# Optimization experiments

Hardware: AMD Instinct MI355X
Metric: run time of the kernel (lower is better)

Reference implementation:

```python
import jax, jax.numpy as jnp
import numpy as np

NUM_HEADS = 16
ROPE_THETA = 10000.0


def setup_inputs() -> dict:
    key = jax.random.key(0)
    k1, k2, k3 = jax.random.split(key, 3)
    B, T, C = 2, 2048, 1024
    x = jax.random.normal(k1, (B, T, C), dtype=jnp.float32)
    w_qkv = jax.random.normal(k2, (3 * C, C), dtype=jnp.float32) * 0.02
    w_out = jax.random.normal(k3, (C, C), dtype=jnp.float32) * 0.02
    return {"x": x, "w_qkv": w_qkv, "w_out": w_out}


def _apply_rope(x, cos, sin):
    # x: (B, H, T, D); interleaved complex pairs: (x[...,2i], x[...,2i+1])
    B, H, T, D = x.shape
    xp = x.reshape(B, H, T, D // 2, 2)
    xr, xi = xp[..., 0], xp[..., 1]
    # cos/sin: (T, D//2) broadcast over (B, H)
    out_r = xr * cos - xi * sin
    out_i = xr * sin + xi * cos
    return jnp.stack([out_r, out_i], axis=-1).reshape(B, H, T, D)


def reference(x, w_qkv, w_out):
    B, T, C = x.shape
    H = NUM_HEADS
    D = C // H
    scale = 1.0 / np.sqrt(D).astype(np.float32)

    qkv = x @ w_qkv.T                      # (B, T, 3C)
    q, k, v = jnp.split(qkv, 3, axis=-1)

    def to_heads(t):
        return t.reshape(B, T, H, D).transpose(0, 2, 1, 3)  # (B, H, T, D)

    q, k, v = to_heads(q), to_heads(k), to_heads(v)

    # RoPE frequencies: freqs[t, j] = t / theta^(2j/D)
    inv_freq = 1.0 / (ROPE_THETA ** (jnp.arange(0, D, 2, dtype=jnp.float32) / D))
    freqs = jnp.arange(T, dtype=jnp.float32)[:, None] * inv_freq[None, :]  # (T, D//2)
    cos, sin = jnp.cos(freqs), jnp.sin(freqs)

    q = _apply_rope(q, cos, sin)
    k = _apply_rope(k, cos, sin)

    att = jnp.einsum('bhqd,bhkd->bhqk', q, k) * scale   # (B, H, T, T)
    causal = jnp.tril(jnp.ones((T, T), dtype=bool))
    att = jnp.where(causal[None, None], att, -jnp.inf)
    att = jax.nn.softmax(att, axis=-1)
    # dropout p=0.0 (eval) -> identity

    out = jnp.einsum('bhqk,bhkd->bhqd', att, v)          # (B, H, T, D)
    out = out.transpose(0, 2, 1, 3).reshape(B, T, C)
    return out @ w_out.T
```

## Files before the change

kernel.cpp:

```cpp
#include <hip/hip_runtime.h>
#include <hip/hip_bf16.h>
#include <math.h>

#define DEV __device__ __forceinline__

typedef float  floatx4 __attribute__((ext_vector_type(4)));
typedef short  bf16x8  __attribute__((ext_vector_type(8)));
typedef short  bf16x4  __attribute__((ext_vector_type(4)));

typedef __attribute__((address_space(1))) void gvoid;
typedef __attribute__((address_space(3))) void lvoid;

static constexpr int Bc = 2, Tc = 2048, Cc = 1024, Hc = 16, Dc = 64;

DEV void gload16(const void* g, void* l) {
    __builtin_amdgcn_global_load_lds((gvoid*)g, (lvoid*)l, 16, 0, 0);
}

__global__ void prep_kernel(const float* __restrict__ xf,
                            const float* __restrict__ wqkvf,
                            const float* __restrict__ woutf,
                            __hip_bfloat16* __restrict__ xb,
                            __hip_bfloat16* __restrict__ wqkvb,
                            __hip_bfloat16* __restrict__ woutb,
                            float* __restrict__ cosT, float* __restrict__ sinT) {
    int gb = blockIdx.x;
    if (gb < 8192) {
        const float* src; __hip_bfloat16* dst; int i;
        if (gb < 4096)      { src = xf;    dst = xb;    i = gb * 256 + threadIdx.x; }
        else if (gb < 7168) { src = wqkvf; dst = wqkvb; i = (gb - 4096) * 256 + threadIdx.x; }
        else                { src = woutf; dst = woutb; i = (gb - 7168) * 256 + threadIdx.x; }
        float4 f = ((const float4*)src)[i];
        union { ushort4 u; __hip_bfloat16 h[4]; } pk;
        pk.h[0] = __float2bfloat16(f.x);
        pk.h[1] = __float2bfloat16(f.y);
        pk.h[2] = __float2bfloat16(f.z);
        pk.h[3] = __float2bfloat16(f.w);
        ((ushort4*)dst)[i] = pk.u;
    } else {
        int i = (gb - 8192) * 256 + threadIdx.x;
        int j = i >> 11, t = i & 2047;
        float invf = powf(10000.0f, -(float)j / 32.0f);
        float f = (float)t * invf;
        cosT[i] = cosf(f);
        sinT[i] = sinf(f);
    }
}

__global__ __launch_bounds__(256, 2) void gemm_qkv(
    const __hip_bfloat16* __restrict__ A,
    const __hip_bfloat16* __restrict__ Bm,
    __hip_bfloat16* __restrict__ qb,
    __hip_bfloat16* __restrict__ kb,
    __hip_bfloat16* __restrict__ vb,
    const float* __restrict__ cosT,
    const float* __restrict__ sinT,
    int K)
{
    __shared__ __align__(16) __hip_bfloat16 SM[2 * 128 * 64];
    __hip_bfloat16* const As = SM;
    __hip_bfloat16* const Bs = SM + 128 * 64;

    const int tid  = threadIdx.x;
    const int lane = tid & 63, wave = tid >> 6;
    const int quad = lane >> 4, cidx = lane & 15;
    const int wm = wave & 1, wn = wave >> 1;
    const int bm = blockIdx.x * 128, bn = blockIdx.y * 128;

    floatx4 acc[4][4] = {};

    for (int k0 = 0; k0 < K; k0 += 64) {
#pragma unroll
        for (int it = 0; it < 4; ++it) {
            int idx = tid + it * 256;
            int r = idx >> 3, cs = idx & 7;
            int cg = cs ^ (r & 7);
            gload16(A  + (size_t)(bm + r) * K + k0 + cg * 8, As + idx * 8);
            gload16(Bm + (size_t)(bn + r) * K + k0 + cg * 8, Bs + idx * 8);
        }
        __syncthreads();
#pragma unroll
        for (int ks = 0; ks < 2; ++ks) {
            bf16x8 af[4], bf[4];
#pragma unroll
            for (int mt = 0; mt < 4; ++mt) {
                int r = wm * 64 + mt * 16 + cidx;
                af[mt] = *(const bf16x8*)(As + (r * 8 + ((ks * 4 + quad) ^ (r & 7))) * 8);
            }
#pragma unroll
            for (int nt = 0; nt < 4; ++nt) {
                int r = wn * 64 + nt * 16 + cidx;
                bf[nt] = *(const bf16x8*)(Bs + (r * 8 + ((ks * 4 + quad) ^ (r & 7))) * 8);
            }
#pragma unroll
            for (int mt = 0; mt < 4; ++mt)
#pragma unroll
                for (int nt = 0; nt < 4; ++nt)
                    acc[mt][nt] = __builtin_amdgcn_mfma_f32_16x16x32_bf16(
                        af[mt], bf[nt], acc[mt][nt], 0, 0, 0);
        }
        __syncthreads();
    }

    if (bn >= 2048) {
#pragma unroll
        for (int nt = 0; nt < 4; ++nt) {
            int n_l = wn * 64 + nt * 16 + cidx;
#pragma unroll
            for (int mt = 0; mt < 4; ++mt)
#pragma unroll
                for (int reg = 0; reg < 4; ++reg) {
                    int m_l = wm * 64 + mt * 16 + quad * 4 + reg;
                    SM[n_l * 128 + (((m_l >> 3) ^ (n_l & 15)) * 8) + (m_l & 7)] =
                        __float2bfloat16(acc[mt][nt][reg]);
                }
        }
        __syncthreads();
        {
            int b = bm >> 11, t0 = bm & 2047;
            int c = tid & 15;
#pragma unroll
            for (int it = 0; it < 8; ++it) {
                int row = it * 16 + (tid >> 4);
                int cc = (bn - 2048) + row;
                int h = cc >> 6, d = cc & 63;
                *(uint4*)(vb + ((size_t)(b * Hc + h) * Dc + d) * Tc + t0 + c * 8) =
                    *(const uint4*)(SM + row * 128 + ((c ^ (row & 15)) * 8));
            }
        }
    } else {
        const float SL2E = 0.125f * 1.44269504088896f;
        const bool isq = (bn < 1024);
#pragma unroll
        for (int nt = 0; nt < 4; ++nt) {
            int n_l = wn * 64 + nt * 16 + cidx;
            int d = n_l & 63, j = d >> 1;
            const float* cp = cosT + j * 2048;
            const float* sp = sinT + j * 2048;
#pragma unroll
            for (int mt = 0; mt < 4; ++mt) {
                int m0 = wm * 64 + mt * 16 + quad * 4;
                int t0 = (bm + m0) & 2047;
                float4 c4 = *(const float4*)(cp + t0);
                float4 s4 = *(const float4*)(sp + t0);
#pragma unroll
                for (int reg = 0; reg < 4; ++reg) {
                    float v = acc[mt][nt][reg];
                    float p = __shfl_xor(v, 1);
                    float cz = ((const float*)&c4)[reg];
                    float sz = ((const float*)&s4)[reg];
                    float o = (d & 1) ? (p * sz + v * cz) : (v * cz - p * sz);
                    if (isq) o *= SL2E;
                    int m_l = m0 + reg;
                    SM[m_l * 128 + (((n_l >> 3) ^ (m_l & 15)) * 8) + (n_l & 7)] =
                        __float2bfloat16(o);
                }
            }
        }
        __syncthreads();
        {
            __hip_bfloat16* dst = isq ? qb : kb;
            const int bnl = bn & 1023;
#pragma unroll
            for (int it = 0; it < 8; ++it) {
                int c = it * 256 + tid;
                int row = c >> 4, s = c & 15;
                int m = bm + row;
                int b = m >> 11, t = m & 2047;
                int h = (bnl >> 6) + (s >> 3);
                int d0 = (s & 7) * 8;
                *(uint4*)(dst + ((size_t)(b * Hc + h) * Tc + t) * Dc + d0) =
                    *(const uint4*)(SM + row * 128 + ((s ^ (row & 15)) * 8));
            }
        }
    }
}

__global__ __launch_bounds__(256, 2) void gemm_out(
    const __hip_bfloat16* __restrict__ A,
    const __hip_bfloat16* __restrict__ Bm,
    float* __restrict__ Cout)
{
    __shared__ __align__(16) __hip_bfloat16 As[64 * 64];
    __shared__ __align__(16) __hip_bfloat16 Bs[128 * 64];

    const int tid  = threadIdx.x;
    const int lane = tid & 63, wave = tid >> 6;
    const int quad = lane >> 4, cidx = lane & 15;
    const int bm = blockIdx.x * 64, bn = blockIdx.y * 128;
    const int K = 1024;

    floatx4 acc[4][2] = {};

    for (int k0 = 0; k0 < K; k0 += 64) {
        int h = k0 >> 6;
#pragma unroll
        for (int it = 0; it < 2; ++it) {
            int idx = tid + it * 256;
            int r = idx >> 3, cs = idx & 7;
            int cg = cs ^ (r & 7);
            int m = bm + r;
            const __hip_bfloat16* src =
                A + ((size_t)((m >> 11) * 16 + h) * 2048 + (m & 2047)) * 64 + cg * 8;
            gload16(src, As + idx * 8);
        }
#pragma unroll
        for (int it = 0; it < 4; ++it) {
            int idx = tid + it * 256;
            int r = idx >> 3, cs = idx & 7;
            int cg = cs ^ (r & 7);
            gload16(Bm + (size_t)(bn + r) * K + k0 + cg * 8, Bs + idx * 8);
        }
        __syncthreads();
#pragma unroll
        for (int ks = 0; ks < 2; ++ks) {
            bf16x8 af[4], bf[2];
#pragma unroll
            for (int mt = 0; mt < 4; ++mt) {
                int r = mt * 16 + cidx;
                af[mt] = *(const bf16x8*)(As + (r * 8 + ((ks * 4 + quad) ^ (r & 7))) * 8);
            }
#pragma unroll
            for (int nt = 0; nt < 2; ++nt) {
                int r = wave * 32 + nt * 16 + cidx;
                bf[nt] = *(const bf16x8*)(Bs + (r * 8 + ((ks * 4 + quad) ^ (r & 7))) * 8);
            }
#pragma unroll
            for (int mt = 0; mt < 4; ++mt)
#pragma unroll
                for (int nt = 0; nt < 2; ++nt)
                    acc[mt][nt] = __builtin_amdgcn_mfma_f32_16x16x32_bf16(
                        af[mt], bf[nt], acc[mt][nt], 0, 0, 0);
        }
        __syncthreads();
    }

#pragma unroll
    for (int mt = 0; mt < 4; ++mt)
#pragma unroll
        for (int nt = 0; nt < 2; ++nt) {
            int n = bn + wave * 32 + nt * 16 + cidx;
#pragma unroll
            for (int reg = 0; reg < 4; ++reg) {
                int m = bm + mt * 16 + quad * 4 + reg;
                Cout[(size_t)m * 1024 + n] = acc[mt][nt][reg];
            }
        }
}

__global__ __launch_bounds__(256, 2) void attn_kernel(
    const __hip_bfloat16* __restrict__ qb,
    const __hip_bfloat16* __restrict__ kb,
    const __hip_bfloat16* __restrict__ vb,
    __hip_bfloat16* __restrict__ ob)
{
    __shared__ __align__(16) __hip_bfloat16 Ks[128 * 64];
    __shared__ __align__(16) __hip_bfloat16 Vt[64 * 128];
    __shared__ __align__(16) __hip_bfloat16 Ps[128 * 64];
    __shared__ float Ls[4][64];

    const int tid  = threadIdx.x;
    const int lane = tid & 63, wave = tid >> 6;
    const int quad = lane >> 4, cidx = lane & 15;
    const int id = blockIdx.x;
    const int xcd = id & 7, s = id >> 3;
    const int bh = xcd * 4 + (s >> 4);
    const int bx = s & 15;
    const size_t plane = (size_t)bh * Tc * Dc;
    const __hip_bfloat16* Vp = vb + plane;
    const __hip_bfloat16* Kp = kb + plane;

    for (int half = 0; half < 2; ++half) {
        const int qt = half ? bx : 31 - bx;
        const int qbase = qt * 64;
        const int ktmax = (qbase + 63) >> 7;

#pragma unroll
        for (int it = 0; it < 2; ++it) {
            int idx = tid + it * 256;
            int r = idx >> 3, cs = idx & 7;
            int cg = cs ^ (r & 7);
            gload16(qb + plane + (size_t)(qbase + r) * 64 + cg * 8, Ks + idx * 8);
        }
        __syncthreads();
        bf16x8 qf[4][2];
#pragma unroll
        for (int mt = 0; mt < 4; ++mt)
#pragma unroll
            for (int ks = 0; ks < 2; ++ks) {
                int r = mt * 16 + cidx;
                qf[mt][ks] = *(const bf16x8*)(Ks + (r * 8 + ((ks * 4 + quad) ^ (r & 7))) * 8);
            }
        __syncthreads();

        floatx4 oaccT[4][4] = {};
        float lsum[4] = {0.f, 0.f, 0.f, 0.f};

        for (int kt = 0; kt <= ktmax; ++kt) {
            bf16x8 kcur[2][2];
#pragma unroll
            for (int nt2 = 0; nt2 < 2; ++nt2)
#pragma unroll
                for (int ks = 0; ks < 2; ++ks)
                    kcur[nt2][ks] = *(const bf16x8*)(
                        Kp + (size_t)(kt * 128 + wave * 32 + nt2 * 16 + cidx) * 64
                           + (ks * 4 + quad) * 8);

#pragma unroll
            for (int it = 0; it < 4; ++it) {
                int idx = tid + it * 256;
                int r = idx >> 4, cs = idx & 15;
                int c = cs ^ (r & 15);
                gload16(Vp + (size_t)r * Tc + kt * 128 + c * 8, Vt + idx * 8);
            }

            floatx4 sacc[4][2] = {};
#pragma unroll
            for (int ks = 0; ks < 2; ++ks)
#pragma unroll
                for (int mt = 0; mt < 4; ++mt)
#pragma unroll
                    for (int nt2 = 0; nt2 < 2; ++nt2)
                        sacc[mt][nt2] = __builtin_amdgcn_mfma_f32_16x16x32_bf16(
                            kcur[nt2][ks], qf[mt][ks], sacc[mt][nt2], 0, 0, 0);

            const bool domask = (kt == ktmax);
            bf16x4 pf[4][2];
#pragma unroll
            for (int mt = 0; mt < 4; ++mt) {
                int q = qbase + mt * 16 + cidx;
#pragma unroll
                for (int nt2 = 0; nt2 < 2; ++nt2) {
#pragma unroll
                    for (int reg = 0; reg < 4; ++reg) {
                        int key = kt * 128 + wave * 32 + nt2 * 16 + quad * 4 + reg;
                        float p = __builtin_amdgcn_exp2f(sacc[mt][nt2][reg]);
                        if (domask && key > q) p = 0.0f;
                        lsum[mt] += p;
                        __hip_bfloat16 hb = __float2bfloat16(p);
                        pf[mt][nt2][reg] = *(const short*)&hb;
                    }
                }
            }

            __syncthreads();

#pragma unroll
            for (int dt = 0; dt < 4; ++dt) {
                int d = dt * 16 + cidx;
#pragma unroll
                for (int ks2 = 0; ks2 < 2; ++ks2) {
                    int chunk = wave * 4 + ks2 * 2 + (quad >> 1);
                    bf16x4 vtf = *(const bf16x4*)(
                        Vt + (d * 16 + (chunk ^ (d & 15))) * 8 + (quad & 1) * 4);
#pragma unroll
                    for (int mt = 0; mt < 4; ++mt)
                        oaccT[mt][dt] = __builtin_amdgcn_mfma_f32_16x16x16bf16_1k(
                            vtf, pf[mt][ks2], oaccT[mt][dt], 0, 0, 0);
                }
            }
            __syncthreads();
        }

#pragma unroll
        for (int off = 16; off < 64; off <<= 1)
#pragma unroll
            for (int mt = 0; mt < 4; ++mt)
                lsum[mt] += __shfl_xor(lsum[mt], off);
        if (quad == 0)
#pragma unroll
            for (int mt = 0; mt < 4; ++mt)
                Ls[wave][mt * 16 + cidx] = lsum[mt];

        if (wave != 0) {
            float* dstw = (wave == 1) ? (float*)Ks : (wave == 2) ? (float*)Vt : (float*)Ps;
#pragma unroll
            for (int mt = 0; mt < 4; ++mt)
#pragma unroll
                for (int dt = 0; dt < 4; ++dt)
                    ((floatx4*)dstw)[(mt * 4 + dt) * 64 + lane] = oaccT[mt][dt];
        }
        __syncthreads();
        if (wave == 0) {
#pragma unroll
            for (int mt = 0; mt < 4; ++mt)
#pragma unroll
                for (int dt = 0; dt < 4; ++dt) {
                    int i = (mt * 4 + dt) * 64 + lane;
                    oaccT[mt][dt] += ((const floatx4*)Ks)[i];
                    oaccT[mt][dt] += ((const floatx4*)Vt)[i];
                    oaccT[mt][dt] += ((const floatx4*)Ps)[i];
                }
#pragma unroll
            for (int mt = 0; mt < 4; ++mt) {
                int q = mt * 16 + cidx;
                float lt = Ls[0][q] + Ls[1][q] + Ls[2][q] + Ls[3][q];
                float inv = 1.0f / lt;
#pragma unroll
                for (int dt = 0; dt < 4; ++dt) {
                    bf16x4 o4;
#pragma unroll
                    for (int reg = 0; reg < 4; ++reg) {
                        __hip_bfloat16 hb = __float2bfloat16(oaccT[mt][dt][reg] * inv);
                        o4[reg] = *(const short*)&hb;
                    }
                    int g = dt * 4 + quad;
                    *(bf16x4*)(Ps + q * 64 + (g ^ (q & 12)) * 4) = o4;
                }
            }
        }
        __syncthreads();
#pragma unroll
        for (int i = 0; i < 2; ++i) {
            int c = tid * 2 + i;
            int row = c >> 3, cp = c & 7;
            *(uint4*)(ob + plane + (size_t)(qbase + row) * 64 + cp * 8) =
                *(const uint4*)(Ps + row * 64 + ((cp * 2) ^ (row & 12)) * 4);
        }
        __syncthreads();
    }
}

extern "C" void kernel_launch(void* const* d_in, const int* in_sizes, int n_in,
                              void* d_out, int out_size, void* d_ws, size_t ws_size,
                              hipStream_t stream) {
    const float* xf = nullptr; const float* wqkvf = nullptr; const float* woutf = nullptr;
    for (int i = 0; i < n_in; ++i) {
        if      (in_sizes[i] == 2 * 2048 * 1024) xf    = (const float*)d_in[i];
        else if (in_sizes[i] == 3 * 1024 * 1024) wqkvf = (const float*)d_in[i];
        else if (in_sizes[i] == 1024 * 1024)     woutf = (const float*)d_in[i];
    }
    float* out = (float*)d_out;

    char* ws = (char*)d_ws;
    const size_t MB = 1024 * 1024;
    __hip_bfloat16* qb    = (__hip_bfloat16*)(ws);
    __hip_bfloat16* kb    = (__hip_bfloat16*)(ws + 8  * MB);
    __hip_bfloat16* vb    = (__hip_bfloat16*)(ws + 16 * MB);
    __hip_bfloat16* ab    = (__hip_bfloat16*)(ws + 24 * MB);
    float* cosT           = (float*)(ws + 32 * MB);
    float* sinT           = (float*)(ws + 32 * MB + 256 * 1024);
    __hip_bfloat16* xb    = (__hip_bfloat16*)(ws + 33 * MB);
    __hip_bfloat16* wqkvb = (__hip_bfloat16*)(ws + 41 * MB);
    __hip_bfloat16* woutb = (__hip_bfloat16*)(ws + 47 * MB);

    prep_kernel<<<dim3(8448), dim3(256), 0, stream>>>(
        xf, wqkvf, woutf, xb, wqkvb, woutb, cosT, sinT);

    gemm_qkv<<<dim3(32, 24), dim3(256), 0, stream>>>(
        xb, wqkvb, qb, kb, vb, cosT, sinT, 1024);
    attn_kernel<<<dim3(512), dim3(256), 0, stream>>>(qb, kb, vb, ab);
    gemm_out<<<dim3(64, 8), dim3(256), 0, stream>>>(ab, woutb, out);
}
```

Baseline: 161.6 us.

## Swizzle GEMM block order, enlarge out-proj tile, add MFMA priority hints

Both GEMMs now launch a 1D grid and remap block ids in a swizzled order, with the intent of improving L2 reuse of operand tiles across concurrently running blocks. The output-projection GEMM moves from 64x128 to 128x128 tiles with a 2x2 wave layout, which raises per-block data reuse but halves the block count to 256, risking lower occupancy across CUs. The attention kernel wraps its MFMA sections in s_setprio to favor matrix issue over other waves.

```diff
diff --git a/kernel.cpp b/kernel.cpp
--- a/kernel.cpp
+++ b/kernel.cpp
@@ -65,7 +65,9 @@
     const int lane = tid & 63, wave = tid >> 6;
     const int quad = lane >> 4, cidx = lane & 15;
     const int wm = wave & 1, wn = wave >> 1;
-    const int bm = blockIdx.x * 128, bn = blockIdx.y * 128;
+    const int id  = blockIdx.x;
+    const int swz = (id & 7) * 96 + (id >> 3);
+    const int bm = (swz & 31) * 128, bn = (swz >> 5) * 128;
 
     floatx4 acc[4][4] = {};
 
@@ -181,54 +183,51 @@
     const __hip_bfloat16* __restrict__ Bm,
     float* __restrict__ Cout)
 {
-    __shared__ __align__(16) __hip_bfloat16 As[64 * 64];
-    __shared__ __align__(16) __hip_bfloat16 Bs[128 * 64];
+    __shared__ __align__(16) __hip_bfloat16 SM[2 * 128 * 64];
+    __hip_bfloat16* const As = SM;
+    __hip_bfloat16* const Bs = SM + 128 * 64;
 
     const int tid  = threadIdx.x;
     const int lane = tid & 63, wave = tid >> 6;
     const int quad = lane >> 4, cidx = lane & 15;
-    const int bm = blockIdx.x * 64, bn = blockIdx.y * 128;
+    const int wm = wave & 1, wn = wave >> 1;
+    const int id  = blockIdx.x;
+    const int swz = (id & 7) * 32 + (id >> 3);
+    const int bm = (swz & 31) * 128, bn = (swz >> 5) * 128;
     const int K = 1024;
 
-    floatx4 acc[4][2] = {};
+    floatx4 acc[4][4] = {};
 
     for (int k0 = 0; k0 < K; k0 += 64) {
         int h = k0 >> 6;
 #pragma unroll
-        for (int it = 0; it < 2; ++it) {
+        for (int it = 0; it < 4; ++it) {
             int idx = tid + it * 256;
             int r = idx >> 3, cs = idx & 7;
             int cg = cs ^ (r & 7);
             int m = bm + r;
-            const __hip_bfloat16* src =
-                A + ((size_t)((m >> 11) * 16 + h) * 2048 + (m & 2047)) * 64 + cg * 8;
-            gload16(src, As + idx * 8);
-        }
-#pragma unroll
-        for (int it = 0; it < 4; ++it) {
-            int idx = tid + it * 256;
-            int r = idx >> 3, cs = idx & 7;
-            int cg = cs ^ (r & 7);
+            gload16(A + ((size_t)((m >> 11) * 16 + h) * 2048 + (m & 2047)) * 64 + cg * 8,
+                    As + idx * 8);
             gload16(Bm + (size_t)(bn + r) * K + k0 + cg * 8, Bs + idx * 8);
         }
         __syncthreads();
 #pragma unroll
         for (int ks = 0; ks < 2; ++ks) {
-            bf16x8 af[4], bf[2];
+            bf16x8 af[4], bf[4];
 #pragma unroll
             for (int mt = 0; mt < 4; ++mt) {
-                int r = mt * 16 + cidx;
+                int r = wm * 64 + mt * 16 + cidx;
                 af[mt] = *(const bf16x8*)(As + (r * 8 + ((ks * 4 + quad) ^ (r & 7))) * 8);
             }
 #pragma unroll
-            for (int nt = 0; nt < 2; ++nt) {
-                int r = wave * 32 + nt * 16 + cidx;
+            for (int nt = 0; nt < 4; ++nt) {
+                int r = wn * 64 + nt * 16 + cidx;
                 bf[nt] = *(const bf16x8*)(Bs + (r * 8 + ((ks * 4 + quad) ^ (r & 7))) * 8);
             }
 #pragma unroll
             for (int mt = 0; mt < 4; ++mt)
 #pragma unroll
-                for (int nt = 0; nt < 2; ++nt)
+                for (int nt = 0; nt < 4; ++nt)
                     acc[mt][nt] = __builtin_amdgcn_mfma_f32_16x16x32_bf16(
                         af[mt], bf[nt], acc[mt][nt], 0, 0, 0);
         }
@@ -238,11 +237,11 @@
 #pragma unroll
     for (int mt = 0; mt < 4; ++mt)
 #pragma unroll
-        for (int nt = 0; nt < 2; ++nt) {
-            int n = bn + wave * 32 + nt * 16 + cidx;
+        for (int nt = 0; nt < 4; ++nt) {
+            int n = bn + wn * 64 + nt * 16 + cidx;
 #pragma unroll
             for (int reg = 0; reg < 4; ++reg) {
-                int m = bm + mt * 16 + quad * 4 + reg;
+                int m = bm + wm * 64 + mt * 16 + quad * 4 + reg;
                 Cout[(size_t)m * 1024 + n] = acc[mt][nt][reg];
             }
         }
@@ -315,6 +314,7 @@
             }
 
             floatx4 sacc[4][2] = {};
+            __builtin_amdgcn_s_setprio(1);
 #pragma unroll
             for (int ks = 0; ks < 2; ++ks)
 #pragma unroll
@@ -323,6 +323,7 @@
                     for (int nt2 = 0; nt2 < 2; ++nt2)
                         sacc[mt][nt2] = __builtin_amdgcn_mfma_f32_16x16x32_bf16(
                             kcur[nt2][ks], qf[mt][ks], sacc[mt][nt2], 0, 0, 0);
+            __builtin_amdgcn_s_setprio(0);
 
             const bool domask = (kt == ktmax);
             bf16x4 pf[4][2];
@@ -345,6 +346,7 @@
 
             __syncthreads();
 
+            __builtin_amdgcn_s_setprio(1);
 #pragma unroll
             for (int dt = 0; dt < 4; ++dt) {
                 int d = dt * 16 + cidx;
@@ -359,6 +361,7 @@
                             vtf, pf[mt][ks2], oaccT[mt][dt], 0, 0, 0);
                 }
             }
+            __builtin_amdgcn_s_setprio(0);
             __syncthreads();
         }
 
@@ -447,8 +450,8 @@
     prep_kernel<<<dim3(8448), dim3(256), 0, stream>>>(
         xf, wqkvf, woutf, xb, wqkvb, woutb, cosT, sinT);
 
-    gemm_qkv<<<dim3(32, 24), dim3(256), 0, stream>>>(
+    gemm_qkv<<<dim3(768), dim3(256), 0, stream>>>(
         xb, wqkvb, qb, kb, vb, cosT, sinT, 1024);
     attn_kernel<<<dim3(512), dim3(256), 0, stream>>>(qb, kb, vb, ab);
-    gemm_out<<<dim3(64, 8), dim3(256), 0, stream>>>(ab, woutb, out);
-}
+    gemm_out<<<dim3(256), dim3(256), 0, stream>>>(ab, woutb, out);
+}
```

Result: slower. 174.5 us (+8.0%).
